# Kernel tuning notes

Hardware: AMD Instinct MI355X
Metric: run time of the kernel (lower is better)

## Reference

```python
import jax, jax.numpy as jnp
import numpy as np

BS = 32768
NIN = 512
E = 8          # num_experts
T = 2          # num_tasks
H = 256        # num_neurons_expert
NT = 1         # num_neurons_tower


def setup_inputs() -> dict:
    key = jax.random.key(0)
    ks = jax.random.split(key, 7)
    s_in = 1.0 / np.sqrt(NIN)
    s_h = 1.0 / np.sqrt(H)
    return {
        "xv": jax.random.normal(ks[0], (BS, NIN), dtype=jnp.float32),
        "We": jax.random.uniform(ks[1], (E, NIN, H), dtype=jnp.float32, minval=-s_in, maxval=s_in),
        "be": jax.random.uniform(ks[2], (E, H), dtype=jnp.float32, minval=-s_in, maxval=s_in),
        "Wg": jax.random.uniform(ks[3], (T, NIN, E), dtype=jnp.float32, minval=-s_in, maxval=s_in),
        "bg": jax.random.uniform(ks[4], (T, E), dtype=jnp.float32, minval=-s_in, maxval=s_in),
        "Wt": jax.random.uniform(ks[5], (T, H, NT), dtype=jnp.float32, minval=-s_h, maxval=s_h),
        "bt": jax.random.uniform(ks[6], (T, NT), dtype=jnp.float32, minval=-s_h, maxval=s_h),
        "bs": BS,
    }


def reference(xv, We, be, Wg, bg, Wt, bt, bs):
    # Experts: [bs, E, H] (dropout is identity in eval mode)
    out_experts = jax.nn.relu(jnp.einsum("bi,eih->beh", xv, We) + be[None, :, :])
    # Gates: [bs, T, E], softmax over experts
    gates = jax.nn.softmax(jnp.einsum("bi,tie->bte", xv, Wg) + bg[None, :, :], axis=-1)
    # Gated combine: [bs, T, H]
    input_towers = jnp.einsum("bte,beh->bth", gates, out_experts)
    # Towers: [bs, T, NT] -> squeeze NT=1 -> [bs, T]
    out_towers = jax.nn.relu(jnp.einsum("bth,thn->btn", input_towers, Wt) + bt[None, :, :])
    out = jax.nn.sigmoid(out_towers[:, :, 0])  # [bs, T]
    return (out[:, 0], out[:, 1])
```

## Files before the change

kernel.cpp:

```cpp
#include <hip/hip_runtime.h>

typedef __attribute__((ext_vector_type(8))) short short8;
typedef __attribute__((ext_vector_type(4))) float floatx4;
typedef __attribute__((ext_vector_type(4))) float f32x4;

#define BS   32768

__device__ __forceinline__ unsigned short f2bf(float f) {
  unsigned int u = __float_as_uint(f);
  u += 0x7fffu + ((u >> 16) & 1u);
  return (unsigned short)(u >> 16);
}

__global__ void prep_weT(const float* __restrict__ We, unsigned short* __restrict__ WeT) {
  int e  = blockIdx.x >> 6;
  int kc = blockIdx.x & 63;
  int h  = threadIdx.x;
  short8 pk;
#pragma unroll
  for (int j = 0; j < 8; ++j)
    pk[j] = (short)f2bf(We[e * 131072 + (kc * 8 + j) * 256 + h]);
  *reinterpret_cast<short8*>(&WeT[e * 131072 + h * 512 + kc * 8]) = pk;
}

__global__ void prep_wgT(const float* __restrict__ Wg, unsigned short* __restrict__ WgT) {
  int row = blockIdx.x;
  int t = row >> 3, e = row & 7;
  int lane = threadIdx.x;
  short8 pk;
#pragma unroll
  for (int j = 0; j < 8; ++j)
    pk[j] = (short)f2bf(Wg[t * 4096 + (lane * 8 + j) * 8 + e]);
  *reinterpret_cast<short8*>(&WgT[row * 512 + lane * 8]) = pk;
}

#define GLOAD16(SRC, DST) \
  __builtin_amdgcn_global_load_lds( \
      (const __attribute__((address_space(1))) unsigned int*)(SRC), \
      (__attribute__((address_space(3))) unsigned int*)(DST), 16, 0, 0)

__global__ __launch_bounds__(256) void conv_gates(
    const float* __restrict__ xv, const unsigned short* __restrict__ WgT,
    const float* __restrict__ bg, unsigned short* __restrict__ Abf,
    float* __restrict__ gates_ws)
{
  __shared__ __attribute__((aligned(16))) unsigned char bufA[65536];
  const int tid = threadIdx.x;
  const int b0  = blockIdx.x * 64;
  const int r8 = tid >> 3, kslot = tid & 7;
  const int mt = b0 >> 8;
  const int rc_base = b0 & 255;
  unsigned char* AbfB = reinterpret_cast<unsigned char*>(Abf);

#pragma unroll
  for (int pass = 0; pass < 2; ++pass) {
    int r = pass * 32 + r8;
    int r_c = rc_base + r;
    const float* xrow = xv + (size_t)(b0 + r) * 512;
    unsigned swz = (unsigned)((r & 7) << 4);
#pragma unroll
    for (int j = 0; j < 8; ++j) {
      int o = j * 8 + kslot;
      f32x4 v0 = *reinterpret_cast<const f32x4*>(xrow + o * 8);
      f32x4 v1 = *reinterpret_cast<const f32x4*>(xrow + o * 8 + 4);
      short8 pk;
      pk[0] = (short)f2bf(v0[0]); pk[1] = (short)f2bf(v0[1]);
      pk[2] = (short)f2bf(v0[2]); pk[3] = (short)f2bf(v0[3]);
      pk[4] = (short)f2bf(v1[0]); pk[5] = (short)f2bf(v1[1]);
      pk[6] = (short)f2bf(v1[2]); pk[7] = (short)f2bf(v1[3]);
      unsigned lb = ((unsigned)r << 10) + (((unsigned)(o * 16)) ^ swz);
      *reinterpret_cast<short8*>(&bufA[lb]) = pk;
      unsigned gb = (unsigned)((mt * 8 + j) * 32768) + (unsigned)(r_c * 128)
                  + (((unsigned)(kslot * 16)) ^ swz);
      *reinterpret_cast<short8*>(&AbfB[gb]) = pk;
    }
  }
  __syncthreads();

  const int wave = tid >> 6, lane = tid & 63;
  const int row16 = lane & 15, kgrp = lane >> 4;
  floatx4 gacc = {0.f, 0.f, 0.f, 0.f};
  const unsigned abase = ((unsigned)row16 << 10) + ((unsigned)kgrp << 4) + ((unsigned)wave << 14);
  const unsigned a_swz = (unsigned)((row16 & 7) << 4);
  const unsigned short* wg_lane = WgT + row16 * 512 + kgrp * 8;
#pragma unroll
  for (int ks = 0; ks < 16; ++ks) {
    short8 af = *reinterpret_cast<const short8*>(&bufA[(abase + (unsigned)(ks << 6)) ^ a_swz]);
    short8 bf = *reinterpret_cast<const short8*>(wg_lane + ks * 32);
    gacc = __builtin_amdgcn_mfma_f32_16x16x32_bf16(af, bf, gacc, 0, 0, 0);
  }
  float bgv = bg[row16];
#pragma unroll
  for (int j = 0; j < 4; ++j) {
    float v = gacc[j] + bgv;
    float mx = v;
    mx = fmaxf(mx, __shfl_xor(mx, 1));
    mx = fmaxf(mx, __shfl_xor(mx, 2));
    mx = fmaxf(mx, __shfl_xor(mx, 4));
    float p = __expf(v - mx);
    float s = p;
    s += __shfl_xor(s, 1);
    s += __shfl_xor(s, 2);
    s += __shfl_xor(s, 4);
    gates_ws[row16 * BS + b0 + wave * 16 + kgrp * 4 + j] = p / s;
  }
}

__global__ __launch_bounds__(512, 2) void mmoe_main(
    const unsigned short* __restrict__ Abf,
    const unsigned short* __restrict__ WeT,
    const float* __restrict__ gates_ws,
    const float* __restrict__ be,
    const float* __restrict__ Wt,
    float* __restrict__ acc_ws)
{
  __shared__ __attribute__((aligned(16))) unsigned char smem[131072];
  __shared__ float red_lds[4][256][2];

  const int tid = threadIdx.x, wave = tid >> 6, lane = tid & 63;
  const int row16 = lane & 15, kgrp = lane >> 4;
  const int wm = wave >> 2, wn = wave & 3;
  const int bid = blockIdx.x;
  const int e = bid >> 7, mt = bid & 127;

  const unsigned short* Asrc = Abf + (size_t)mt * 131072;
  const unsigned short* Bsrc = WeT + e * 131072;

  unsigned soffB[4];
#pragma unroll
  for (int i = 0; i < 4; ++i) {
    unsigned x = (unsigned)(i * 8192 + tid * 16);
    unsigned r = x >> 7;
    unsigned y = (x & 127u) ^ ((r & 7u) << 4);
    soffB[i] = r * 512u + (y >> 1);
  }
  const unsigned soffA0 = (unsigned)(tid * 8);

  unsigned char* Ab0 = smem;
  unsigned char* Ab1 = smem + 32768;
  unsigned char* Bb0 = smem + 65536;
  unsigned char* Bb1 = smem + 98304;

#pragma unroll
  for (int i = 0; i < 4; ++i)
    GLOAD16(Asrc + (i * 4096 + soffA0), Ab0 + (i * 8 + wave) * 1024);
#pragma unroll
  for (int i = 0; i < 4; ++i)
    GLOAD16(Bsrc + soffB[i], Bb0 + (i * 8 + wave) * 1024);

  floatx4 acc[8][4];
#pragma unroll
  for (int mf = 0; mf < 8; ++mf)
#pragma unroll
    for (int n = 0; n < 4; ++n) acc[mf][n] = (floatx4){0.f, 0.f, 0.f, 0.f};

  const unsigned swz  = (unsigned)((row16 & 7) << 4);
  const unsigned bcol = (unsigned)(wn * 64 + row16);
  const unsigned arow = (unsigned)(wm * 128 + row16);

#define RDA(AB, MF, KS) \
  (*reinterpret_cast<const short8*>( \
      &(AB)[(arow + (unsigned)((MF) * 16)) * 128 + (((unsigned)((KS) * 64 + kgrp * 16)) ^ swz)]))

#define MFMA4(ACC, AV, BV) \
  _Pragma("unroll") \
  for (int n = 0; n < 4; ++n) \
    ACC[n] = __builtin_amdgcn_mfma_f32_16x16x32_bf16(AV, BV[n], ACC[n], 0, 0, 0);

#pragma unroll
  for (int kt = 0; kt < 8; ++kt) {
    const unsigned char* ab = (kt & 1) ? Ab1 : Ab0;
    const unsigned char* bb = (kt & 1) ? Bb1 : Bb0;
    unsigned char* an = (kt & 1) ? Ab0 : Ab1;
    unsigned char* bn = (kt & 1) ? Bb0 : Bb1;
    const unsigned short* aNext = Asrc + (kt + 1) * 16384;
    const unsigned short* bNext = Bsrc + (kt + 1) * 64;

    if (kt < 7) {
#pragma unroll
      for (int i = 0; i < 4; ++i)
        GLOAD16(aNext + (i * 4096 + soffA0), an + (i * 8 + wave) * 1024);
#pragma unroll
      for (int i = 0; i < 4; ++i)
        GLOAD16(bNext + soffB[i], bn + (i * 8 + wave) * 1024);
      asm volatile("s_waitcnt vmcnt(8)" ::: "memory");
    } else {
      asm volatile("s_waitcnt vmcnt(0)" ::: "memory");
    }
    __builtin_amdgcn_s_barrier();
    __builtin_amdgcn_sched_barrier(0);

    short8 bf[2][4];
#pragma unroll
    for (int ks = 0; ks < 2; ++ks)
#pragma unroll
      for (int n = 0; n < 4; ++n)
        bf[ks][n] = *reinterpret_cast<const short8*>(
            &bb[(bcol + (unsigned)(n * 16)) * 128 + (((unsigned)(ks * 64 + kgrp * 16)) ^ swz)]);
    short8 a00 = RDA(ab, 0, 0), a01 = RDA(ab, 0, 1);
    short8 a10 = RDA(ab, 1, 0), a11 = RDA(ab, 1, 1);
    short8 b00 = RDA(ab, 2, 0), b01 = RDA(ab, 2, 1);
    short8 b10 = RDA(ab, 3, 0), b11 = RDA(ab, 3, 1);
    asm volatile("s_waitcnt lgkmcnt(4)" ::: "memory");
    __builtin_amdgcn_sched_barrier(0);
    __builtin_amdgcn_s_setprio(1);
    MFMA4(acc[0], a00, bf[0]); MFMA4(acc[0], a01, bf[1]);
    MFMA4(acc[1], a10, bf[0]); MFMA4(acc[1], a11, bf[1]);
    __builtin_amdgcn_s_setprio(0);

    short8 c00 = RDA(ab, 4, 0), c01 = RDA(ab, 4, 1);
    short8 c10 = RDA(ab, 5, 0), c11 = RDA(ab, 5, 1);
    asm volatile("s_waitcnt lgkmcnt(4)" ::: "memory");
    __builtin_amdgcn_sched_barrier(0);
    __builtin_amdgcn_s_setprio(1);
    MFMA4(acc[2], b00, bf[0]); MFMA4(acc[2], b01, bf[1]);
    MFMA4(acc[3], b10, bf[0]); MFMA4(acc[3], b11, bf[1]);
    __builtin_amdgcn_s_setprio(0);

    short8 d00 = RDA(ab, 6, 0), d01 = RDA(ab, 6, 1);
    short8 d10 = RDA(ab, 7, 0), d11 = RDA(ab, 7, 1);
    asm volatile("s_waitcnt lgkmcnt(4)" ::: "memory");
    __builtin_amdgcn_sched_barrier(0);
    __builtin_amdgcn_s_setprio(1);
    MFMA4(acc[4], c00, bf[0]); MFMA4(acc[4], c01, bf[1]);
    MFMA4(acc[5], c10, bf[0]); MFMA4(acc[5], c11, bf[1]);
    __builtin_amdgcn_s_setprio(0);

    asm volatile("s_waitcnt lgkmcnt(0)" ::: "memory");
    __builtin_amdgcn_sched_barrier(0);
    __builtin_amdgcn_s_setprio(1);
    MFMA4(acc[6], d00, bf[0]); MFMA4(acc[6], d01, bf[1]);
    MFMA4(acc[7], d10, bf[0]); MFMA4(acc[7], d11, bf[1]);
    __builtin_amdgcn_s_setprio(0);
    __builtin_amdgcn_s_barrier();
    __builtin_amdgcn_sched_barrier(0);
  }
#undef RDA
#undef MFMA4

  float bev[4], wtv[2][4];
#pragma unroll
  for (int n = 0; n < 4; ++n) bev[n] = be[e * 256 + wn * 64 + n * 16 + row16];
#pragma unroll
  for (int t = 0; t < 2; ++t)
#pragma unroll
    for (int n = 0; n < 4; ++n) wtv[t][n] = Wt[t * 256 + wn * 64 + n * 16 + row16];

#pragma unroll
  for (int mf = 0; mf < 8; ++mf) {
#pragma unroll
    for (int j = 0; j < 4; ++j) {
      float p0 = 0.f, p1 = 0.f;
#pragma unroll
      for (int n = 0; n < 4; ++n) {
        float r = fmaxf(acc[mf][n][j] + bev[n], 0.f);
        p0 = fmaf(r, wtv[0][n], p0);
        p1 = fmaf(r, wtv[1][n], p1);
      }
      p0 += __shfl_xor(p0, 1); p1 += __shfl_xor(p1, 1);
      p0 += __shfl_xor(p0, 2); p1 += __shfl_xor(p1, 2);
      p0 += __shfl_xor(p0, 4); p1 += __shfl_xor(p1, 4);
      p0 += __shfl_xor(p0, 8); p1 += __shfl_xor(p1, 8);
      if (row16 == 0) {
        int rw = wm * 128 + mf * 16 + kgrp * 4 + j;
        red_lds[wn][rw][0] = p0;
        red_lds[wn][rw][1] = p1;
      }
    }
  }
  __syncthreads();

  {
    int row = tid >> 1, t = tid & 1;
    float s = red_lds[0][row][t] + red_lds[1][row][t]
            + red_lds[2][row][t] + red_lds[3][row][t];
    float g = gates_ws[(t * 8 + e) * BS + mt * 256 + row];
    atomicAdd(&acc_ws[t * BS + mt * 256 + row], s * g);
  }
}

__global__ void finalize(const float* __restrict__ acc_ws, const float* __restrict__ bt,
                         float* __restrict__ out) {
  int i = blockIdx.x * 256 + threadIdx.x;
  int t = i >> 15;
  float s = fmaxf(acc_ws[i] + bt[t], 0.f);
  out[i] = 1.f / (1.f + __expf(-s));
}

extern "C" void kernel_launch(void* const* d_in, const int* in_sizes, int n_in,
                              void* d_out, int out_size, void* d_ws, size_t ws_size,
                              hipStream_t stream) {
  const float* xv = (const float*)d_in[0];
  const float* We = (const float*)d_in[1];
  const float* be = (const float*)d_in[2];
  const float* Wg = (const float*)d_in[3];
  const float* bg = (const float*)d_in[4];
  const float* Wt = (const float*)d_in[5];
  const float* bt = (const float*)d_in[6];
  float* out = (float*)d_out;

  unsigned char* ws = (unsigned char*)d_ws;
  unsigned short* WeT      = (unsigned short*)(ws);
  unsigned short* WgT      = (unsigned short*)(ws + (2u << 20));
  unsigned short* Abf      = (unsigned short*)(ws + (4u << 20));
  float*          gates_ws = (float*)(ws + (36u << 20));
  float*          acc_ws   = (float*)(ws + (38u << 20));

  hipMemsetAsync(acc_ws, 0, 2 * BS * sizeof(float), stream);
  prep_weT<<<512, 256, 0, stream>>>(We, WeT);
  prep_wgT<<<16, 64, 0, stream>>>(Wg, WgT);
  conv_gates<<<512, 256, 0, stream>>>(xv, WgT, bg, Abf, gates_ws);
  mmoe_main<<<1024, 512, 0, stream>>>(Abf, WeT, gates_ws, be, Wt, acc_ws);
  finalize<<<256, 256, 0, stream>>>(acc_ws, bt, out);
}
```

Before: 121.5 us.

## Switch main GEMM to 32x32x16 MFMA tiles and merge weight prep kernels

Rewrites the expert GEMM inner loop to use 32x32x16 bf16 MFMA instructions with 4x2 fragments per wave instead of 16x16x32 with 8x4 fragments. This cuts the number of LDS fragment reads per k-step and raises operand reuse, but changes the accumulator layout, so the epilogue reduction now needs an extra shuffle stage. The two weight-conversion kernels are also merged into one launch to save launch overhead.

```diff
diff --git a/kernel.cpp b/kernel.cpp
--- a/kernel.cpp
+++ b/kernel.cpp
@@ -2,6 +2,7 @@
 
 typedef __attribute__((ext_vector_type(8))) short short8;
 typedef __attribute__((ext_vector_type(4))) float floatx4;
+typedef __attribute__((ext_vector_type(16))) float floatx16;
 typedef __attribute__((ext_vector_type(4))) float f32x4;
 
 #define BS   32768
@@ -12,26 +13,28 @@
   return (unsigned short)(u >> 16);
 }
 
-__global__ void prep_weT(const float* __restrict__ We, unsigned short* __restrict__ WeT) {
-  int e  = blockIdx.x >> 6;
-  int kc = blockIdx.x & 63;
-  int h  = threadIdx.x;
-  short8 pk;
-#pragma unroll
-  for (int j = 0; j < 8; ++j)
-    pk[j] = (short)f2bf(We[e * 131072 + (kc * 8 + j) * 256 + h]);
-  *reinterpret_cast<short8*>(&WeT[e * 131072 + h * 512 + kc * 8]) = pk;
-}
-
-__global__ void prep_wgT(const float* __restrict__ Wg, unsigned short* __restrict__ WgT) {
-  int row = blockIdx.x;
-  int t = row >> 3, e = row & 7;
-  int lane = threadIdx.x;
-  short8 pk;
-#pragma unroll
-  for (int j = 0; j < 8; ++j)
-    pk[j] = (short)f2bf(Wg[t * 4096 + (lane * 8 + j) * 8 + e]);
-  *reinterpret_cast<short8*>(&WgT[row * 512 + lane * 8]) = pk;
+__global__ void prep_w(const float* __restrict__ We, const float* __restrict__ Wg,
+                       unsigned short* __restrict__ WeT, unsigned short* __restrict__ WgT) {
+  int bid = blockIdx.x;
+  if (bid < 512) {
+    int e  = bid >> 6;
+    int kc = bid & 63;
+    int h  = threadIdx.x;
+    short8 pk;
+#pragma unroll
+    for (int j = 0; j < 8; ++j)
+      pk[j] = (short)f2bf(We[e * 131072 + (kc * 8 + j) * 256 + h]);
+    *reinterpret_cast<short8*>(&WeT[e * 131072 + h * 512 + kc * 8]) = pk;
+  } else if (threadIdx.x < 64) {
+    int row = bid - 512;
+    int t = row >> 3, e = row & 7;
+    int lane = threadIdx.x;
+    short8 pk;
+#pragma unroll
+    for (int j = 0; j < 8; ++j)
+      pk[j] = (short)f2bf(Wg[t * 4096 + (lane * 8 + j) * 8 + e]);
+    *reinterpret_cast<short8*>(&WgT[row * 512 + lane * 8]) = pk;
+  }
 }
 
 #define GLOAD16(SRC, DST) \
@@ -118,7 +121,7 @@
   __shared__ float red_lds[4][256][2];
 
   const int tid = threadIdx.x, wave = tid >> 6, lane = tid & 63;
-  const int row16 = lane & 15, kgrp = lane >> 4;
+  const int l31 = lane & 31, lh = lane >> 5;
   const int wm = wave >> 2, wn = wave & 3;
   const int bid = blockIdx.x;
   const int e = bid >> 7, mt = bid & 127;
@@ -148,24 +151,34 @@
   for (int i = 0; i < 4; ++i)
     GLOAD16(Bsrc + soffB[i], Bb0 + (i * 8 + wave) * 1024);
 
-  floatx4 acc[8][4];
-#pragma unroll
-  for (int mf = 0; mf < 8; ++mf)
-#pragma unroll
-    for (int n = 0; n < 4; ++n) acc[mf][n] = (floatx4){0.f, 0.f, 0.f, 0.f};
-
-  const unsigned swz  = (unsigned)((row16 & 7) << 4);
-  const unsigned bcol = (unsigned)(wn * 64 + row16);
-  const unsigned arow = (unsigned)(wm * 128 + row16);
-
-#define RDA(AB, MF, KS) \
+  floatx16 acc[4][2];
+#pragma unroll
+  for (int mf = 0; mf < 4; ++mf)
+#pragma unroll
+    for (int nf = 0; nf < 2; ++nf)
+#pragma unroll
+      for (int q = 0; q < 16; ++q) acc[mf][nf][q] = 0.f;
+
+  const unsigned arow = (unsigned)(wm * 128);
+  const unsigned bcol = (unsigned)(wn * 64);
+  const unsigned koff0 = (unsigned)(lh * 16);
+
+#define RDF(BUF, ROWBASE, F, KS) \
   (*reinterpret_cast<const short8*>( \
-      &(AB)[(arow + (unsigned)((MF) * 16)) * 128 + (((unsigned)((KS) * 64 + kgrp * 16)) ^ swz)]))
-
-#define MFMA4(ACC, AV, BV) \
+      &(BUF)[((ROWBASE) + (unsigned)((F) * 32) + (unsigned)l31) * 128 + \
+             (((unsigned)((KS) * 32) + koff0) ^ (unsigned)((l31 & 7) << 4))]))
+
+#define RD6(AB, BB, KS, AV, BV) \
+  AV[0] = RDF(AB, arow, 0, KS); AV[1] = RDF(AB, arow, 1, KS); \
+  AV[2] = RDF(AB, arow, 2, KS); AV[3] = RDF(AB, arow, 3, KS); \
+  BV[0] = RDF(BB, bcol, 0, KS); BV[1] = RDF(BB, bcol, 1, KS);
+
+#define MFMA8(AV, BV) \
   _Pragma("unroll") \
-  for (int n = 0; n < 4; ++n) \
-    ACC[n] = __builtin_amdgcn_mfma_f32_16x16x32_bf16(AV, BV[n], ACC[n], 0, 0, 0);
+  for (int mf = 0; mf < 4; ++mf) { \
+    acc[mf][0] = __builtin_amdgcn_mfma_f32_32x32x16_bf16(AV[mf], BV[0], acc[mf][0], 0, 0, 0); \
+    acc[mf][1] = __builtin_amdgcn_mfma_f32_32x32x16_bf16(AV[mf], BV[1], acc[mf][1], 0, 0, 0); \
+  }
 
 #pragma unroll
   for (int kt = 0; kt < 8; ++kt) {
@@ -190,81 +203,68 @@
     __builtin_amdgcn_s_barrier();
     __builtin_amdgcn_sched_barrier(0);
 
-    short8 bf[2][4];
-#pragma unroll
-    for (int ks = 0; ks < 2; ++ks)
-#pragma unroll
-      for (int n = 0; n < 4; ++n)
-        bf[ks][n] = *reinterpret_cast<const short8*>(
-            &bb[(bcol + (unsigned)(n * 16)) * 128 + (((unsigned)(ks * 64 + kgrp * 16)) ^ swz)]);
-    short8 a00 = RDA(ab, 0, 0), a01 = RDA(ab, 0, 1);
-    short8 a10 = RDA(ab, 1, 0), a11 = RDA(ab, 1, 1);
-    short8 b00 = RDA(ab, 2, 0), b01 = RDA(ab, 2, 1);
-    short8 b10 = RDA(ab, 3, 0), b11 = RDA(ab, 3, 1);
-    asm volatile("s_waitcnt lgkmcnt(4)" ::: "memory");
+    short8 av0[4], bv0[2], av1[4], bv1[2], av2[4], bv2[2], av3[4], bv3[2];
+    RD6(ab, bb, 0, av0, bv0);
+    RD6(ab, bb, 1, av1, bv1);
+    asm volatile("s_waitcnt lgkmcnt(6)" ::: "memory");
     __builtin_amdgcn_sched_barrier(0);
     __builtin_amdgcn_s_setprio(1);
-    MFMA4(acc[0], a00, bf[0]); MFMA4(acc[0], a01, bf[1]);
-    MFMA4(acc[1], a10, bf[0]); MFMA4(acc[1], a11, bf[1]);
+    MFMA8(av0, bv0);
     __builtin_amdgcn_s_setprio(0);
-
-    short8 c00 = RDA(ab, 4, 0), c01 = RDA(ab, 4, 1);
-    short8 c10 = RDA(ab, 5, 0), c11 = RDA(ab, 5, 1);
-    asm volatile("s_waitcnt lgkmcnt(4)" ::: "memory");
+    RD6(ab, bb, 2, av2, bv2);
+    asm volatile("s_waitcnt lgkmcnt(6)" ::: "memory");
     __builtin_amdgcn_sched_barrier(0);
     __builtin_amdgcn_s_setprio(1);
-    MFMA4(acc[2], b00, bf[0]); MFMA4(acc[2], b01, bf[1]);
-    MFMA4(acc[3], b10, bf[0]); MFMA4(acc[3], b11, bf[1]);
+    MFMA8(av1, bv1);
     __builtin_amdgcn_s_setprio(0);
-
-    short8 d00 = RDA(ab, 6, 0), d01 = RDA(ab, 6, 1);
-    short8 d10 = RDA(ab, 7, 0), d11 = RDA(ab, 7, 1);
-    asm volatile("s_waitcnt lgkmcnt(4)" ::: "memory");
+    RD6(ab, bb, 3, av3, bv3);
+    asm volatile("s_waitcnt lgkmcnt(6)" ::: "memory");
     __builtin_amdgcn_sched_barrier(0);
     __builtin_amdgcn_s_setprio(1);
-    MFMA4(acc[4], c00, bf[0]); MFMA4(acc[4], c01, bf[1]);
-    MFMA4(acc[5], c10, bf[0]); MFMA4(acc[5], c11, bf[1]);
+    MFMA8(av2, bv2);
     __builtin_amdgcn_s_setprio(0);
-
     asm volatile("s_waitcnt lgkmcnt(0)" ::: "memory");
     __builtin_amdgcn_sched_barrier(0);
     __builtin_amdgcn_s_setprio(1);
-    MFMA4(acc[6], d00, bf[0]); MFMA4(acc[6], d01, bf[1]);
-    MFMA4(acc[7], d10, bf[0]); MFMA4(acc[7], d11, bf[1]);
+    MFMA8(av3, bv3);
     __builtin_amdgcn_s_setprio(0);
     __builtin_amdgcn_s_barrier();
     __builtin_amdgcn_sched_barrier(0);
   }
-#undef RDA
-#undef MFMA4
-
-  float bev[4], wtv[2][4];
-#pragma unroll
-  for (int n = 0; n < 4; ++n) bev[n] = be[e * 256 + wn * 64 + n * 16 + row16];
-#pragma unroll
-  for (int t = 0; t < 2; ++t)
-#pragma unroll
-    for (int n = 0; n < 4; ++n) wtv[t][n] = Wt[t * 256 + wn * 64 + n * 16 + row16];
-
-#pragma unroll
-  for (int mf = 0; mf < 8; ++mf) {
-#pragma unroll
-    for (int j = 0; j < 4; ++j) {
-      float p0 = 0.f, p1 = 0.f;
-#pragma unroll
-      for (int n = 0; n < 4; ++n) {
-        float r = fmaxf(acc[mf][n][j] + bev[n], 0.f);
-        p0 = fmaf(r, wtv[0][n], p0);
-        p1 = fmaf(r, wtv[1][n], p1);
+#undef RDF
+#undef RD6
+#undef MFMA8
+
+  float bev[2], wt0[2], wt1[2];
+#pragma unroll
+  for (int nf = 0; nf < 2; ++nf) {
+    int h = wn * 64 + nf * 32 + l31;
+    bev[nf] = be[e * 256 + h];
+    wt0[nf] = Wt[h];
+    wt1[nf] = Wt[256 + h];
+  }
+
+#pragma unroll
+  for (int mf = 0; mf < 4; ++mf) {
+#pragma unroll
+    for (int q = 0; q < 16; ++q) {
+      float s0 = 0.f, s1 = 0.f;
+#pragma unroll
+      for (int nf = 0; nf < 2; ++nf) {
+        float r = fmaxf(acc[mf][nf][q] + bev[nf], 0.f);
+        s0 = fmaf(r, wt0[nf], s0);
+        s1 = fmaf(r, wt1[nf], s1);
       }
-      p0 += __shfl_xor(p0, 1); p1 += __shfl_xor(p1, 1);
-      p0 += __shfl_xor(p0, 2); p1 += __shfl_xor(p1, 2);
-      p0 += __shfl_xor(p0, 4); p1 += __shfl_xor(p1, 4);
-      p0 += __shfl_xor(p0, 8); p1 += __shfl_xor(p1, 8);
-      if (row16 == 0) {
-        int rw = wm * 128 + mf * 16 + kgrp * 4 + j;
-        red_lds[wn][rw][0] = p0;
-        red_lds[wn][rw][1] = p1;
+      s0 += __shfl_xor(s0, 1);  s1 += __shfl_xor(s1, 1);
+      s0 += __shfl_xor(s0, 2);  s1 += __shfl_xor(s1, 2);
+      s0 += __shfl_xor(s0, 4);  s1 += __shfl_xor(s1, 4);
+      s0 += __shfl_xor(s0, 8);  s1 += __shfl_xor(s1, 8);
+      s0 += __shfl_xor(s0, 16); s1 += __shfl_xor(s1, 16);
+      if (l31 == 0) {
+        int rl = (q & 3) + 8 * (q >> 2) + 4 * lh;
+        int row = wm * 128 + mf * 32 + rl;
+        red_lds[wn][row][0] = s0;
+        red_lds[wn][row][1] = s1;
       }
     }
   }
@@ -307,8 +307,7 @@
   float*          acc_ws   = (float*)(ws + (38u << 20));
 
   hipMemsetAsync(acc_ws, 0, 2 * BS * sizeof(float), stream);
-  prep_weT<<<512, 256, 0, stream>>>(We, WeT);
-  prep_wgT<<<16, 64, 0, stream>>>(Wg, WgT);
+  prep_w<<<528, 256, 0, stream>>>(We, Wg, WeT, WgT);
   conv_gates<<<512, 256, 0, stream>>>(xv, WgT, bg, Abf, gates_ws);
   mmoe_main<<<1024, 512, 0, stream>>>(Abf, WeT, gates_ws, be, Wt, acc_ws);
   finalize<<<256, 256, 0, stream>>>(acc_ws, bt, out);
```

New measurement: 157.4 us. +29.6%, slower.
